# Kernel optimization log

Hardware: AMD Instinct MI355X
Metric: run time of the kernel (lower is better)

## Reference

```python
import jax, jax.numpy as jnp
import numpy as np

BOX_SIZE = 256
POS_ENC_DIM = 10


def positional_encoding_geom2(coords, enc_dim, DD):
    # coords: [..., 3] -> [..., 3*enc_dim*2]
    D2 = DD // 2
    i = jnp.arange(enc_dim, dtype=coords.dtype)
    freqs = D2 * (1.0 / D2) ** (i / (enc_dim - 1))  # [enc_dim]
    k = coords[..., None] * freqs  # [..., 3, enc_dim]
    x = jnp.concatenate([jnp.sin(k), jnp.cos(k)], axis=-1)  # [..., 3, 2*enc_dim]
    return x.reshape(*x.shape[:-2], -1)


def setup_inputs() -> dict:
    key = jax.random.key(0)
    ks = jax.random.split(key, 6)
    B, N, L, H, n_layers = 8, 50000, 32, 128, 6
    in_dim = 3 * POS_ENC_DIM * 2 + L  # 92
    return {
        "z0": jax.random.normal(ks[0], (B, L), dtype=jnp.float32),
        "cons": jax.random.uniform(ks[1], (N, 3), dtype=jnp.float32),
        "w_lin0": jax.random.normal(ks[2], (H, in_dim), dtype=jnp.float32) * (in_dim ** -0.5),
        "w_deform": jax.random.normal(ks[3], (n_layers, H, H), dtype=jnp.float32) * (H ** -0.5),
        "w_lin1a": jax.random.normal(ks[4], (3, H), dtype=jnp.float32) * (H ** -0.5),
        "w_lin1b": jax.random.normal(ks[5], (3, 3), dtype=jnp.float32) * 0.1,
    }


def reference(z0, cons, w_lin0, w_deform, w_lin1a, w_lin1b):
    B = z0.shape[0]
    N = cons.shape[0]
    # positional encoding of consensus points: [N, 60]
    cons_pos = positional_encoding_geom2(cons, POS_ENC_DIM, BOX_SIZE)
    posi = jnp.broadcast_to(cons, (B, N, 3))
    posi_n = jnp.broadcast_to(cons_pos, (B, N, cons_pos.shape[-1]))
    conf_feat = jnp.broadcast_to(z0[:, None, :], (B, N, z0.shape[-1]))
    x = jnp.concatenate([posi_n, conf_feat], axis=2)  # [B, N, 92]
    # lin0 (bias-free) -> deform stack of ELU(Linear) blocks
    x = jnp.einsum('bnf,of->bno', x, w_lin0)  # [B, N, H]
    for j in range(w_deform.shape[0]):
        x = jax.nn.elu(jnp.einsum('bnh,oh->bno', x, w_deform[j]))
    res = jax.nn.elu(jnp.einsum('bnh,oh->bno', x, w_lin1a))  # [B, N, 3]
    res = jnp.einsum('bni,oi->bno', res, w_lin1b)  # [B, N, 3]
    pos = posi + res
    resn = res
    return (pos, resn)
```

## Files before the change

kernel.cpp:

```cpp
#include <hip/hip_runtime.h>
#include <hip/hip_bf16.h>
#include <math.h>

typedef _Float16 half8 __attribute__((ext_vector_type(8)));
typedef float    f32x4 __attribute__((ext_vector_type(4)));

#define NPTS  50000
#define BATCH 8
#define PT 2

__global__ void prep_weights_k(const float* __restrict__ w_lin0,
                               const float* __restrict__ w_def,
                               const float* __restrict__ w1a,
                               _Float16* __restrict__ W)
{
    int idx = blockIdx.x * blockDim.x + threadIdx.x;
    if (idx >= 8*128*128) return;
    int slot = idx >> 14;
    int r    = idx & 16383;
    int ft   = r >> 11;
    int ks   = (r >> 9) & 3;
    int lane = (r >> 3) & 63;
    int j    = r & 7;
    int p = lane & 15, g = lane >> 4;
    int o = ft*16 + p;
    int k = ks*32 + 16*(j>>2) + 4*g + (j&3);
    float v = 0.f;
    if (slot == 0) {
        if (k < 60)                 v = w_lin0[o*92 + k];
        else if (k >= 64 && k < 96) v = w_lin0[o*92 + 60 + (k-64)];
    } else if (slot <= 6) {
        v = w_def[(slot-1)*16384 + o*128 + k];
    } else {
        if (o < 3) v = w1a[o*128 + k];
    }
    W[idx] = (_Float16)v;
}

__device__ __forceinline__ float elu1(float v) {
    return (v > 0.f) ? v : (__expf(v) - 1.f);
}

template<int NKS, bool DOELU>
__device__ __forceinline__ void layer_step(const unsigned char* __restrict__ Wl,
                                           const unsigned char* __restrict__ Wnext,
                                           const half8 (&Bin)[PT][4],
                                           half8 (&Bout)[PT][4],
                                           half8 (&A)[2][4],
                                           int voff)
{
    const f32x4 Z = {0.f, 0.f, 0.f, 0.f};
    f32x4 acc[2][PT][2];
    #pragma unroll
    for (int ft = 0; ft < 8; ++ft) {
        const int cur = ft & 1, nxt = cur ^ 1;
        const unsigned char* pbase = (ft < 7) ? (Wl + (ft+1)*4096) : Wnext;
        #pragma unroll
        for (int ks = 0; ks < 4; ++ks)
            A[nxt][ks] = *(const half8*)(pbase + voff + ks*1024);

        const int pr = ft >> 1;
        const int as = pr & 1;
        const int f  = ft & 1;
        #pragma unroll
        for (int pt = 0; pt < PT; ++pt) {
            f32x4 a = __builtin_amdgcn_mfma_f32_16x16x32_f16(
                A[cur][0], Bin[pt][0], Z, 0, 0, 0);
            #pragma unroll
            for (int ks = 1; ks < NKS; ++ks)
                a = __builtin_amdgcn_mfma_f32_16x16x32_f16(
                    A[cur][ks], Bin[pt][ks], a, 0, 0, 0);
            acc[as][pt][f] = a;
        }
        if (f == 0 && pr >= 1) {
            #pragma unroll
            for (int pt = 0; pt < PT; ++pt) {
                half8 h;
                #pragma unroll
                for (int q = 0; q < 4; ++q) {
                    float v0 = acc[as^1][pt][0][q];
                    float v1 = acc[as^1][pt][1][q];
                    if (DOELU) { v0 = elu1(v0); v1 = elu1(v1); }
                    h[q]   = (_Float16)v0;
                    h[4+q] = (_Float16)v1;
                }
                Bout[pt][pr-1] = h;
            }
        }
    }
    #pragma unroll
    for (int pt = 0; pt < PT; ++pt) {
        half8 h;
        #pragma unroll
        for (int q = 0; q < 4; ++q) {
            float v0 = acc[1][pt][0][q];
            float v1 = acc[1][pt][1][q];
            if (DOELU) { v0 = elu1(v0); v1 = elu1(v1); }
            h[q]   = (_Float16)v0;
            h[4+q] = (_Float16)v1;
        }
        Bout[pt][3] = h;
    }
}

__global__ __launch_bounds__(256, 3)
void decoder_main(const float* __restrict__ z0,
                  const float* __restrict__ cons,
                  const _Float16* __restrict__ W,
                  const float* __restrict__ w1b,
                  float* __restrict__ out)
{
    const int lane = threadIdx.x & 63;
    const int wid  = threadIdx.x >> 6;
    const int p = lane & 15;
    const int g = lane >> 4;
    const int n0 = blockIdx.x * 16 + wid * 4;
    const int voff = lane * 16;

    const f32x4 Z = {0.f, 0.f, 0.f, 0.f};
    const unsigned char* Wb = (const unsigned char*)W;

    half8 A[2][4];
    #pragma unroll
    for (int ks = 0; ks < 4; ++ks)
        A[0][ks] = *(const half8*)(Wb + voff + ks*1024);

    half8 B1[PT][4], B2[PT][4];
    #pragma unroll
    for (int pt = 0; pt < PT; ++pt) {
        const int lrow = pt*16 + p;
        const int n = n0 + (lrow >> 3);
        const int b = lrow & 7;
        float c0 = cons[n*3+0], c1 = cons[n*3+1], c2 = cons[n*3+2];
        #pragma unroll
        for (int ks = 0; ks < 2; ++ks) {
            half8 h;
            #pragma unroll
            for (int j = 0; j < 8; ++j) {
                int k = ks*32 + 16*(j>>2) + 4*g + (j&3);
                float v = 0.f;
                if (k < 60) {
                    int c = k/20, rem = k%20, i = rem%10;
                    float f  = exp2f(7.f * (1.f - (float)i * (1.f/9.f)));
                    float cc = (c == 0) ? c0 : (c == 1) ? c1 : c2;
                    float a  = cc * f;
                    v = (rem < 10) ? __sinf(a) : __cosf(a);
                }
                h[j] = (_Float16)v;
            }
            B1[pt][ks] = h;
        }
        half8 hz;
        #pragma unroll
        for (int j = 0; j < 8; ++j)
            hz[j] = (_Float16)z0[b*32 + 16*(j>>2) + 4*g + (j&3)];
        B1[pt][2] = hz;
    }

    layer_step<3, false>(Wb,           Wb + 1*32768, B1, B2, A, voff);
    layer_step<4, true >(Wb + 1*32768, Wb + 2*32768, B2, B1, A, voff);
    layer_step<4, true >(Wb + 2*32768, Wb + 3*32768, B1, B2, A, voff);
    layer_step<4, true >(Wb + 3*32768, Wb + 4*32768, B2, B1, A, voff);
    layer_step<4, true >(Wb + 4*32768, Wb + 5*32768, B1, B2, A, voff);
    layer_step<4, true >(Wb + 5*32768, Wb + 6*32768, B2, B1, A, voff);
    layer_step<4, true >(Wb + 6*32768, Wb + 7*32768, B1, B2, A, voff);

    f32x4 a1[PT];
    {
        #pragma unroll
        for (int pt = 0; pt < PT; ++pt)
            a1[pt] = __builtin_amdgcn_mfma_f32_16x16x32_f16(A[0][0], B2[pt][0], Z, 0, 0, 0);
        #pragma unroll
        for (int ks = 1; ks < 4; ++ks)
            #pragma unroll
            for (int pt = 0; pt < PT; ++pt)
                a1[pt] = __builtin_amdgcn_mfma_f32_16x16x32_f16(A[0][ks], B2[pt][ks], a1[pt], 0, 0, 0);
    }

    if (g == 0) {
        float b00=w1b[0],b01=w1b[1],b02=w1b[2];
        float b10=w1b[3],b11=w1b[4],b12=w1b[5];
        float b20=w1b[6],b21=w1b[7],b22=w1b[8];
        #pragma unroll
        for (int pt = 0; pt < PT; ++pt) {
            int row = pt*16 + p;
            int n = n0 + (row >> 3);
            int b = row & 7;
            float r0 = elu1(a1[pt][0]);
            float r1 = elu1(a1[pt][1]);
            float r2 = elu1(a1[pt][2]);
            int obase = (b*NPTS + n)*3;
            float rv0 = b00*r0 + b01*r1 + b02*r2;
            float rv1 = b10*r0 + b11*r1 + b12*r2;
            float rv2 = b20*r0 + b21*r1 + b22*r2;
            out[obase+0] = cons[n*3+0] + rv0;
            out[obase+1] = cons[n*3+1] + rv1;
            out[obase+2] = cons[n*3+2] + rv2;
            out[BATCH*NPTS*3 + obase+0] = rv0;
            out[BATCH*NPTS*3 + obase+1] = rv1;
            out[BATCH*NPTS*3 + obase+2] = rv2;
        }
    }
}

extern "C" void kernel_launch(void* const* d_in, const int* in_sizes, int n_in,
                              void* d_out, int out_size, void* d_ws, size_t ws_size,
                              hipStream_t stream)
{
    const float* z0     = (const float*)d_in[0];
    const float* cons   = (const float*)d_in[1];
    const float* w_lin0 = (const float*)d_in[2];
    const float* w_def  = (const float*)d_in[3];
    const float* w1a    = (const float*)d_in[4];
    const float* w1b    = (const float*)d_in[5];
    _Float16* W = (_Float16*)d_ws;

    prep_weights_k<<<512, 256, 0, stream>>>(w_lin0, w_def, w1a, W);
    decoder_main<<<NPTS/16, 256, 0, stream>>>(z0, cons, W, w1b, (float*)d_out);
}
```

Measured before the change: 182.5 us.

## Triple-buffer weight fragments, pack f16 via cvt_pkrtz, pre-swizzle z0 in prep

Weight fragments now go through a three-slot register ring that prefetches two feature tiles ahead instead of one, so global/L2 load latency has more MFMA work to hide behind. MFMA bursts are wrapped in s_setprio to favor matrix issue across waves. The fp32-to-f16 packing uses v_cvt_pkrtz_f16_f32 inline asm, which rounds toward zero rather than to nearest. z0 is pre-converted to half in the required lane layout by the prep kernel, so each thread does one vector load instead of eight scalar loads and converts. The extra buffer adds about 16 VGPRs per thread, which could threaten the 3-waves launch bound or cause spills.

```diff
diff --git a/kernel.cpp b/kernel.cpp
--- a/kernel.cpp
+++ b/kernel.cpp
@@ -2,8 +2,8 @@
 #include <hip/hip_bf16.h>
 #include <math.h>
 
-typedef _Float16 half8 __attribute__((ext_vector_type(8)));
-typedef float    f32x4 __attribute__((ext_vector_type(4)));
+typedef _Float16 half8  __attribute__((ext_vector_type(8)));
+typedef float    f32x4  __attribute__((ext_vector_type(4)));
 
 #define NPTS  50000
 #define BATCH 8
@@ -12,56 +12,77 @@
 __global__ void prep_weights_k(const float* __restrict__ w_lin0,
                                const float* __restrict__ w_def,
                                const float* __restrict__ w1a,
+                               const float* __restrict__ z0,
                                _Float16* __restrict__ W)
 {
     int idx = blockIdx.x * blockDim.x + threadIdx.x;
-    if (idx >= 8*128*128) return;
-    int slot = idx >> 14;
-    int r    = idx & 16383;
-    int ft   = r >> 11;
-    int ks   = (r >> 9) & 3;
-    int lane = (r >> 3) & 63;
-    int j    = r & 7;
-    int p = lane & 15, g = lane >> 4;
-    int o = ft*16 + p;
-    int k = ks*32 + 16*(j>>2) + 4*g + (j&3);
-    float v = 0.f;
-    if (slot == 0) {
-        if (k < 60)                 v = w_lin0[o*92 + k];
-        else if (k >= 64 && k < 96) v = w_lin0[o*92 + 60 + (k-64)];
-    } else if (slot <= 6) {
-        v = w_def[(slot-1)*16384 + o*128 + k];
-    } else {
-        if (o < 3) v = w1a[o*128 + k];
-    }
-    W[idx] = (_Float16)v;
+    if (idx < 8*128*128) {
+        int slot = idx >> 14;
+        int r    = idx & 16383;
+        int ft   = r >> 11;
+        int ks   = (r >> 9) & 3;
+        int lane = (r >> 3) & 63;
+        int j    = r & 7;
+        int p = lane & 15, g = lane >> 4;
+        int o = ft*16 + p;
+        int k = ks*32 + 16*(j>>2) + 4*g + (j&3);
+        float v = 0.f;
+        if (slot == 0) {
+            if (k < 60)                 v = w_lin0[o*92 + k];
+            else if (k >= 64 && k < 96) v = w_lin0[o*92 + 60 + (k-64)];
+        } else if (slot <= 6) {
+            v = w_def[(slot-1)*16384 + o*128 + k];
+        } else {
+            if (o < 3) v = w1a[o*128 + k];
+        }
+        W[idx] = (_Float16)v;
+    } else if (idx < 8*128*128 + 256) {
+        int zi = idx - 8*128*128;
+        int b = zi >> 5, pos = zi & 31, g = pos >> 3, j = pos & 7;
+        W[8*16384 + b*32 + pos] = (_Float16)z0[b*32 + 16*(j>>2) + 4*g + (j&3)];
+    }
 }
 
 __device__ __forceinline__ float elu1(float v) {
     return (v > 0.f) ? v : (__expf(v) - 1.f);
 }
 
-template<int NKS, bool DOELU>
+template<bool DOELU>
+__device__ __forceinline__ half8 pack_pair(f32x4 e, f32x4 o) {
+    if (DOELU) {
+        #pragma unroll
+        for (int q = 0; q < 4; ++q) { e[q] = elu1(e[q]); o[q] = elu1(o[q]); }
+    }
+    union { half8 h; unsigned int u[4]; } u;
+    asm("v_cvt_pkrtz_f16_f32 %0, %1, %2" : "=v"(u.u[0]) : "v"(e[0]), "v"(e[1]));
+    asm("v_cvt_pkrtz_f16_f32 %0, %1, %2" : "=v"(u.u[1]) : "v"(e[2]), "v"(e[3]));
+    asm("v_cvt_pkrtz_f16_f32 %0, %1, %2" : "=v"(u.u[2]) : "v"(o[0]), "v"(o[1]));
+    asm("v_cvt_pkrtz_f16_f32 %0, %1, %2" : "=v"(u.u[3]) : "v"(o[2]), "v"(o[3]));
+    return u.h;
+}
+
+template<int NKS, bool DOELU, int R>
 __device__ __forceinline__ void layer_step(const unsigned char* __restrict__ Wl,
                                            const unsigned char* __restrict__ Wnext,
                                            const half8 (&Bin)[PT][4],
                                            half8 (&Bout)[PT][4],
-                                           half8 (&A)[2][4],
+                                           half8 (&A)[3][4],
                                            int voff)
 {
     const f32x4 Z = {0.f, 0.f, 0.f, 0.f};
     f32x4 acc[2][PT][2];
     #pragma unroll
     for (int ft = 0; ft < 8; ++ft) {
-        const int cur = ft & 1, nxt = cur ^ 1;
-        const unsigned char* pbase = (ft < 7) ? (Wl + (ft+1)*4096) : Wnext;
+        const int cur = (R + ft) % 3;
+        const int pf  = (R + ft + 2) % 3;
+        const unsigned char* pbase = (ft < 6) ? (Wl + (ft+2)*4096)
+                                              : (Wnext + (ft-6)*4096);
         #pragma unroll
         for (int ks = 0; ks < 4; ++ks)
-            A[nxt][ks] = *(const half8*)(pbase + voff + ks*1024);
-
-        const int pr = ft >> 1;
-        const int as = pr & 1;
-        const int f  = ft & 1;
+            A[pf][ks] = *(const half8*)(pbase + voff + ks*1024);
+
+        const int pr = ft >> 1, as = pr & 1, f = ft & 1;
+        __builtin_amdgcn_s_setprio(1);
         #pragma unroll
         for (int pt = 0; pt < PT; ++pt) {
             f32x4 a = __builtin_amdgcn_mfma_f32_16x16x32_f16(
@@ -72,35 +93,16 @@
                     A[cur][ks], Bin[pt][ks], a, 0, 0, 0);
             acc[as][pt][f] = a;
         }
+        __builtin_amdgcn_s_setprio(0);
         if (f == 0 && pr >= 1) {
             #pragma unroll
-            for (int pt = 0; pt < PT; ++pt) {
-                half8 h;
-                #pragma unroll
-                for (int q = 0; q < 4; ++q) {
-                    float v0 = acc[as^1][pt][0][q];
-                    float v1 = acc[as^1][pt][1][q];
-                    if (DOELU) { v0 = elu1(v0); v1 = elu1(v1); }
-                    h[q]   = (_Float16)v0;
-                    h[4+q] = (_Float16)v1;
-                }
-                Bout[pt][pr-1] = h;
-            }
-        }
-    }
-    #pragma unroll
-    for (int pt = 0; pt < PT; ++pt) {
-        half8 h;
-        #pragma unroll
-        for (int q = 0; q < 4; ++q) {
-            float v0 = acc[1][pt][0][q];
-            float v1 = acc[1][pt][1][q];
-            if (DOELU) { v0 = elu1(v0); v1 = elu1(v1); }
-            h[q]   = (_Float16)v0;
-            h[4+q] = (_Float16)v1;
-        }
-        Bout[pt][3] = h;
-    }
+            for (int pt = 0; pt < PT; ++pt)
+                Bout[pt][pr-1] = pack_pair<DOELU>(acc[as^1][pt][0], acc[as^1][pt][1]);
+        }
+    }
+    #pragma unroll
+    for (int pt = 0; pt < PT; ++pt)
+        Bout[pt][3] = pack_pair<DOELU>(acc[1][pt][0], acc[1][pt][1]);
 }
 
 __global__ __launch_bounds__(256, 3)
@@ -120,17 +122,24 @@
     const f32x4 Z = {0.f, 0.f, 0.f, 0.f};
     const unsigned char* Wb = (const unsigned char*)W;
 
-    half8 A[2][4];
-    #pragma unroll
-    for (int ks = 0; ks < 4; ++ks)
+    half8 A[3][4];
+    #pragma unroll
+    for (int ks = 0; ks < 4; ++ks) {
         A[0][ks] = *(const half8*)(Wb + voff + ks*1024);
+        A[1][ks] = *(const half8*)(Wb + 4096 + voff + ks*1024);
+    }
 
     half8 B1[PT][4], B2[PT][4];
+    {
+        const unsigned char* zt = (const unsigned char*)(W + 8*16384);
+        half8 hz = *(const half8*)(zt + (p & 7)*64 + g*16);
+        B1[0][2] = hz;
+        B1[1][2] = hz;
+    }
     #pragma unroll
     for (int pt = 0; pt < PT; ++pt) {
         const int lrow = pt*16 + p;
         const int n = n0 + (lrow >> 3);
-        const int b = lrow & 7;
         float c0 = cons[n*3+0], c1 = cons[n*3+1], c2 = cons[n*3+2];
         #pragma unroll
         for (int ks = 0; ks < 2; ++ks) {
@@ -150,31 +159,26 @@
             }
             B1[pt][ks] = h;
         }
-        half8 hz;
-        #pragma unroll
-        for (int j = 0; j < 8; ++j)
-            hz[j] = (_Float16)z0[b*32 + 16*(j>>2) + 4*g + (j&3)];
-        B1[pt][2] = hz;
-    }
-
-    layer_step<3, false>(Wb,           Wb + 1*32768, B1, B2, A, voff);
-    layer_step<4, true >(Wb + 1*32768, Wb + 2*32768, B2, B1, A, voff);
-    layer_step<4, true >(Wb + 2*32768, Wb + 3*32768, B1, B2, A, voff);
-    layer_step<4, true >(Wb + 3*32768, Wb + 4*32768, B2, B1, A, voff);
-    layer_step<4, true >(Wb + 4*32768, Wb + 5*32768, B1, B2, A, voff);
-    layer_step<4, true >(Wb + 5*32768, Wb + 6*32768, B2, B1, A, voff);
-    layer_step<4, true >(Wb + 6*32768, Wb + 7*32768, B1, B2, A, voff);
+    }
+
+    layer_step<3, false, 0>(Wb,           Wb + 1*32768, B1, B2, A, voff);
+    layer_step<4, true,  2>(Wb + 1*32768, Wb + 2*32768, B2, B1, A, voff);
+    layer_step<4, true,  1>(Wb + 2*32768, Wb + 3*32768, B1, B2, A, voff);
+    layer_step<4, true,  0>(Wb + 3*32768, Wb + 4*32768, B2, B1, A, voff);
+    layer_step<4, true,  2>(Wb + 4*32768, Wb + 5*32768, B1, B2, A, voff);
+    layer_step<4, true,  1>(Wb + 5*32768, Wb + 6*32768, B2, B1, A, voff);
+    layer_step<4, true,  0>(Wb + 6*32768, Wb + 7*32768, B1, B2, A, voff);
 
     f32x4 a1[PT];
     {
         #pragma unroll
         for (int pt = 0; pt < PT; ++pt)
-            a1[pt] = __builtin_amdgcn_mfma_f32_16x16x32_f16(A[0][0], B2[pt][0], Z, 0, 0, 0);
+            a1[pt] = __builtin_amdgcn_mfma_f32_16x16x32_f16(A[2][0], B2[pt][0], Z, 0, 0, 0);
         #pragma unroll
         for (int ks = 1; ks < 4; ++ks)
             #pragma unroll
             for (int pt = 0; pt < PT; ++pt)
-                a1[pt] = __builtin_amdgcn_mfma_f32_16x16x32_f16(A[0][ks], B2[pt][ks], a1[pt], 0, 0, 0);
+                a1[pt] = __builtin_amdgcn_mfma_f32_16x16x32_f16(A[2][ks], B2[pt][ks], a1[pt], 0, 0, 0);
     }
 
     if (g == 0) {
@@ -215,6 +219,6 @@
     const float* w1b    = (const float*)d_in[5];
     _Float16* W = (_Float16*)d_ws;
 
-    prep_weights_k<<<512, 256, 0, stream>>>(w_lin0, w_def, w1a, W);
+    prep_weights_k<<<513, 256, 0, stream>>>(w_lin0, w_def, w1a, z0, W);
     decoder_main<<<NPTS/16, 256, 0, stream>>>(z0, cons, W, w1b, (float*)d_out);
 }
```

Result: faster. 176.1 us (-3.5%).
